# Kernel tuning notes

Measured on AMD Instinct MI355X. Metric: run time of the kernel, lower is better.

Reference implementation:

```python
import jax, jax.numpy as jnp
import numpy as np

EMB = 512      # emb_s * head_cnt = 64 * 8
EMB_S = 64     # scale uses sqrt(emb_s), not sqrt(emb) (quirk of source)
FF = 4 * EMB
LN_EPS = 1e-5


def layer_norm(x, g, b):
    mu = jnp.mean(x, axis=-1, keepdims=True)
    var = jnp.var(x, axis=-1, keepdims=True)
    return (x - mu) * jax.lax.rsqrt(var + LN_EPS) * g + b


def setup_inputs() -> dict:
    key = jax.random.key(0)
    ks = jax.random.split(key, 12)
    B, T = 512, 128
    s = 1.0 / np.sqrt(EMB)
    sf = 1.0 / np.sqrt(FF)
    return {
        "x": jax.random.normal(ks[0], (B, T, EMB), dtype=jnp.float32),
        "wq": jax.random.normal(ks[1], (EMB, EMB), dtype=jnp.float32) * s,
        "bq": jnp.zeros((EMB,), jnp.float32),
        "wk": jax.random.normal(ks[2], (EMB, EMB), dtype=jnp.float32) * s,
        "bk": jnp.zeros((EMB,), jnp.float32),
        "wv": jax.random.normal(ks[3], (EMB, EMB), dtype=jnp.float32) * s,
        "bv": jnp.zeros((EMB,), jnp.float32),
        "g1": jnp.ones((EMB,), jnp.float32),
        "b1": jnp.zeros((EMB,), jnp.float32),
        "g2": jnp.ones((EMB,), jnp.float32),
        "b2": jnp.zeros((EMB,), jnp.float32),
        "w1": jax.random.normal(ks[4], (EMB, FF), dtype=jnp.float32) * s,
        "bm1": jnp.zeros((FF,), jnp.float32),
        "w2": jax.random.normal(ks[5], (FF, EMB), dtype=jnp.float32) * sf,
        "bm2": jnp.zeros((EMB,), jnp.float32),
    }


def reference(x, wq, bq, wk, bk, wv, bv, g1, b1, g2, b2, w1, bm1, w2, bm2):
    B, T, E = x.shape
    # --- attention sub-block (single-head over full emb, per source forward) ---
    h = layer_norm(x, g1, b1)
    q = h @ wq + bq          # [B,T,E]
    k = h @ wk + bk
    v = h @ wv + bv
    att = jnp.einsum("bte,bse->bts", q, k) * (1.0 / np.sqrt(EMB_S))
    causal = jnp.tril(jnp.ones((T, T), dtype=bool))
    att = jnp.where(causal[None, :, :], att, -jnp.inf)
    att = jax.nn.softmax(att, axis=-1)
    y = jnp.einsum("bts,bse->bte", att, v)
    x = x + y  # note: no output projection / dropout on the forward path
    # --- MLP sub-block (dropout is identity in eval) ---
    h2 = layer_norm(x, g2, b2)
    m = jax.nn.gelu(h2 @ w1 + bm1, approximate=False) @ w2 + bm2
    return x + m
```

## Files before the change

kernel.cpp:

```cpp
#include <hip/hip_runtime.h>
#include <hip/hip_bf16.h>
#include <math.h>

typedef __attribute__((ext_vector_type(8))) short s16x8;
typedef __attribute__((ext_vector_type(4))) float f32x4;

static __device__ __forceinline__ float b2f(unsigned short u) {
    union { unsigned int u; float f; } x; x.u = ((unsigned int)u) << 16; return x.f;
}
static __device__ __forceinline__ unsigned short f2b(float f) {
    __hip_bfloat16 h = __float2bfloat16(f);
    return *reinterpret_cast<unsigned short*>(&h);
}
static __device__ __forceinline__ float gelu_fast(float x) {
    float s = x * fmaf(x * x, 0.07135481242f, 1.5957691216f);
    float e = __expf(-s);
    return x * __builtin_amdgcn_rcpf(1.0f + e);
}
static __device__ __forceinline__ void gload16(void* lds, const void* g) {
    __builtin_amdgcn_global_load_lds(
        (const __attribute__((address_space(1))) unsigned int*)g,
        (__attribute__((address_space(3))) unsigned int*)lds, 16, 0, 0);
}

__global__ __launch_bounds__(256) void cvt_t_kernel(
    const float* __restrict__ W, unsigned short* __restrict__ Wt, int K, int N)
{
    __shared__ unsigned short tile[32][33];
    int n0 = blockIdx.x * 32, k0 = blockIdx.y * 32;
    int tx = threadIdx.x & 31, ty = threadIdx.x >> 5;
#pragma unroll
    for (int p = 0; p < 32; p += 8)
        tile[tx][ty + p] = f2b(W[(size_t)(k0 + ty + p) * N + n0 + tx]);
    __syncthreads();
#pragma unroll
    for (int p = 0; p < 32; p += 8)
        Wt[(size_t)(n0 + ty + p) * K + k0 + tx] = tile[ty + p][tx];
}

__global__ __launch_bounds__(256) void concat3_kernel(
    const float* __restrict__ a, const float* __restrict__ b,
    const float* __restrict__ c, float* __restrict__ o)
{
    int i = blockIdx.x * 256 + threadIdx.x;
    if (i < 512) { o[i] = a[i]; o[512 + i] = b[i]; o[1024 + i] = c[i]; }
}

__global__ __launch_bounds__(256) void ln_kernel(
    const float* __restrict__ x,
    const float* __restrict__ g,
    const float* __restrict__ b,
    unsigned short* __restrict__ out, int rows)
{
    int row  = blockIdx.x * 4 + (threadIdx.x >> 6);
    int lane = threadIdx.x & 63;
    if (row >= rows) return;
    const float* xr = x + (size_t)row * 512 + lane * 8;
    float4 d0 = *(const float4*)xr;
    float4 d1 = *(const float4*)(xr + 4);
    float v[8] = {d0.x, d0.y, d0.z, d0.w, d1.x, d1.y, d1.z, d1.w};
    float s = 0.f, ss = 0.f;
#pragma unroll
    for (int j = 0; j < 8; ++j) { s += v[j]; ss += v[j] * v[j]; }
#pragma unroll
    for (int o = 32; o > 0; o >>= 1) { s += __shfl_xor(s, o); ss += __shfl_xor(ss, o); }
    float mu   = s * (1.0f / 512.0f);
    float var  = ss * (1.0f / 512.0f) - mu * mu;
    var = fmaxf(var, 0.0f);
    float rstd = rsqrtf(var + 1e-5f);
    float4 g0 = *(const float4*)(g + lane * 8);
    float4 g1 = *(const float4*)(g + lane * 8 + 4);
    float4 b0 = *(const float4*)(b + lane * 8);
    float4 b1 = *(const float4*)(b + lane * 8 + 4);
    float gg[8] = {g0.x, g0.y, g0.z, g0.w, g1.x, g1.y, g1.z, g1.w};
    float bb[8] = {b0.x, b0.y, b0.z, b0.w, b1.x, b1.y, b1.z, b1.w};
    uint4 res; unsigned short* rs = (unsigned short*)&res;
#pragma unroll
    for (int j = 0; j < 8; ++j)
        rs[j] = f2b((v[j] - mu) * rstd * gg[j] + bb[j]);
    *(uint4*)(out + (size_t)row * 512 + lane * 8) = res;
}

__global__ __launch_bounds__(256) void gemm_bt_kernel(
    const unsigned short* __restrict__ A,
    const unsigned short* __restrict__ Bt,
    const float* __restrict__ bias,
    const float* __restrict__ residual,
    void* __restrict__ Cv,
    int M, int N, int K, int act_gelu, int out_f32)
{
    __shared__ unsigned short As[128 * 32];
    __shared__ unsigned short Bs[128 * 32];

    const int tid  = threadIdx.x;
    const int wave = tid >> 6, lane = tid & 63;
    const int quad = lane >> 4, l16 = lane & 15;

    int bx = blockIdx.x, by = blockIdx.y;
    {
        int nwg = gridDim.x * gridDim.y;
        if ((nwg & 7) == 0) {
            int lid = by * gridDim.x + bx;
            int cpx = nwg >> 3;
            lid = (lid & 7) * cpx + (lid >> 3);
            bx = lid % gridDim.x;
            by = lid / gridDim.x;
        }
    }
    const int bm = by * 128, bn = bx * 128;
    const int wm = (wave >> 1) * 64, wn = (wave & 1) * 64;

    const int srow = 16 * wave + (lane >> 2);
    const int sgrp = (lane & 3) ^ ((srow >> 1) & 3);
    const unsigned short* a_src = A  + (size_t)(bm + srow) * K + sgrp * 8;
    const unsigned short* b_src = Bt + (size_t)(bn + srow) * K + sgrp * 8;
    const size_t rowskip = (size_t)64 * K;
    unsigned short* ldsA = As + 512 * wave;
    unsigned short* ldsB = Bs + 512 * wave;

    const int axor = ((quad ^ ((l16 >> 1) & 3)) * 8);

    f32x4 acc[4][4] = {};

    for (int k0 = 0; k0 < K; k0 += 32) {
        gload16(ldsA,        a_src + k0);
        gload16(ldsA + 2048, a_src + rowskip + k0);
        gload16(ldsB,        b_src + k0);
        gload16(ldsB + 2048, b_src + rowskip + k0);
        __syncthreads();

        s16x8 af[4], bfr[4];
#pragma unroll
        for (int i = 0; i < 4; ++i)
            af[i] = *(const s16x8*)&As[(wm + i * 16 + l16) * 32 + axor];
#pragma unroll
        for (int j = 0; j < 4; ++j)
            bfr[j] = *(const s16x8*)&Bs[(wn + j * 16 + l16) * 32 + axor];
#pragma unroll
        for (int i = 0; i < 4; ++i)
#pragma unroll
            for (int j = 0; j < 4; ++j)
                acc[i][j] = __builtin_amdgcn_mfma_f32_16x16x32_bf16(af[i], bfr[j], acc[i][j], 0, 0, 0);
        __syncthreads();
    }

#pragma unroll
    for (int i = 0; i < 4; ++i) {
#pragma unroll
        for (int j = 0; j < 4; ++j) {
#pragma unroll
            for (int r = 0; r < 4; ++r) {
                int row = bm + wm + i * 16 + quad * 4 + r;
                int col = bn + wn + j * 16 + l16;
                float val = acc[i][j][r] + bias[col];
                if (act_gelu) val = gelu_fast(val);
                if (residual) val += residual[(size_t)row * N + col];
                if (out_f32) ((float*)Cv)[(size_t)row * N + col] = val;
                else ((unsigned short*)Cv)[(size_t)row * N + col] = f2b(val);
            }
        }
    }
}

__global__ __launch_bounds__(256) void attn_kernel(
    const unsigned short* __restrict__ qkv,
    const float* __restrict__ x,
    float* __restrict__ x2)
{
    __shared__ unsigned short Ps[128][128];
    __shared__ unsigned short Vs[64][128];

    int b = blockIdx.x;
    int tid = threadIdx.x;
    int wave = tid >> 6, lane = tid & 63;
    int quad = lane >> 4, l16 = lane & 15;
    const unsigned short* qb = qkv + (size_t)b * 128 * 1536;
    const size_t bo = (size_t)b * 128 * 512;

    f32x4 acc[2][8] = {};
    for (int e0 = 0; e0 < 512; e0 += 32) {
        s16x8 a0 = *(const s16x8*)(qb + (size_t)(wave * 32 + l16) * 1536 + e0 + quad * 8);
        s16x8 a1 = *(const s16x8*)(qb + (size_t)(wave * 32 + 16 + l16) * 1536 + e0 + quad * 8);
#pragma unroll
        for (int j = 0; j < 8; ++j) {
            s16x8 bf = *(const s16x8*)(qb + (size_t)(j * 16 + l16) * 1536 + 512 + e0 + quad * 8);
            acc[0][j] = __builtin_amdgcn_mfma_f32_16x16x32_bf16(a0, bf, acc[0][j], 0, 0, 0);
            acc[1][j] = __builtin_amdgcn_mfma_f32_16x16x32_bf16(a1, bf, acc[1][j], 0, 0, 0);
        }
    }

    const float NEG = -1e30f;
#pragma unroll
    for (int i = 0; i < 2; ++i) {
#pragma unroll
        for (int r = 0; r < 4; ++r) {
            int t = wave * 32 + i * 16 + quad * 4 + r;
            float m = NEG;
#pragma unroll
            for (int j = 0; j < 8; ++j) {
                int s_col = j * 16 + l16;
                float val = acc[i][j][r] * 0.125f;
                val = (s_col <= t) ? val : NEG;
                acc[i][j][r] = val;
                m = fmaxf(m, val);
            }
            for (int o = 1; o < 16; o <<= 1) m = fmaxf(m, __shfl_xor(m, o));
            float sm = 0.f;
#pragma unroll
            for (int j = 0; j < 8; ++j) {
                float e = __expf(acc[i][j][r] - m);
                acc[i][j][r] = e;
                sm += e;
            }
            for (int o = 1; o < 16; o <<= 1) sm += __shfl_xor(sm, o);
            float inv = 1.0f / sm;
#pragma unroll
            for (int j = 0; j < 8; ++j) {
                int g = (j * 2 + (l16 >> 3)) ^ (t & 7);
                Ps[t][g * 8 + (l16 & 7)] = f2b(acc[i][j][r] * inv);
            }
        }
    }
    __syncthreads();

    const float* xb = x + bo;
    float* ob = x2 + bo;
    for (int e0 = 0; e0 < 512; e0 += 64) {
        if (e0) __syncthreads();
#pragma unroll
        for (int p = 0; p < 4; ++p) {
            int s = (tid >> 3) + p * 32;
            int c = (tid & 7) * 8;
            uint4 d = *(const uint4*)(qb + (size_t)s * 1536 + 1024 + e0 + c);
            const unsigned short* dsv = (const unsigned short*)&d;
#pragma unroll
            for (int j = 0; j < 8; ++j) {
                int rr = c + j;
                int g = (s >> 3) ^ j ^ (tid & 7);
                Vs[rr][g * 8 + (s & 7)] = dsv[j];
            }
        }
        __syncthreads();

        f32x4 acc2[2][4] = {};
#pragma unroll
        for (int ks = 0; ks < 4; ++ks) {
            int gp = ((ks * 4 + quad) ^ (l16 & 7)) * 8;
            s16x8 a0 = *(const s16x8*)(&Ps[wave * 32 + l16][gp]);
            s16x8 a1 = *(const s16x8*)(&Ps[wave * 32 + 16 + l16][gp]);
#pragma unroll
            for (int n = 0; n < 4; ++n) {
                int gv = ((ks * 4 + quad) ^ (l16 & 7) ^ ((2 * n + (l16 >> 3)) & 7)) * 8;
                s16x8 bf = *(const s16x8*)(&Vs[n * 16 + l16][gv]);
                acc2[0][n] = __builtin_amdgcn_mfma_f32_16x16x32_bf16(a0, bf, acc2[0][n], 0, 0, 0);
                acc2[1][n] = __builtin_amdgcn_mfma_f32_16x16x32_bf16(a1, bf, acc2[1][n], 0, 0, 0);
            }
        }
#pragma unroll
        for (int i = 0; i < 2; ++i) {
#pragma unroll
            for (int n = 0; n < 4; ++n) {
#pragma unroll
                for (int r = 0; r < 4; ++r) {
                    int t = wave * 32 + i * 16 + quad * 4 + r;
                    int e = e0 + n * 16 + l16;
                    ob[(size_t)t * 512 + e] = acc2[i][n][r] + xb[(size_t)t * 512 + e];
                }
            }
        }
    }
}

extern "C" void kernel_launch(void* const* d_in, const int* in_sizes, int n_in,
                              void* d_out, int out_size, void* d_ws, size_t ws_size,
                              hipStream_t stream) {
    const float* x   = (const float*)d_in[0];
    const float* wq  = (const float*)d_in[1];
    const float* bq  = (const float*)d_in[2];
    const float* wk  = (const float*)d_in[3];
    const float* bk  = (const float*)d_in[4];
    const float* wv  = (const float*)d_in[5];
    const float* bv  = (const float*)d_in[6];
    const float* g1  = (const float*)d_in[7];
    const float* b1  = (const float*)d_in[8];
    const float* g2  = (const float*)d_in[9];
    const float* b2  = (const float*)d_in[10];
    const float* w1  = (const float*)d_in[11];
    const float* bm1 = (const float*)d_in[12];
    const float* w2  = (const float*)d_in[13];
    const float* bm2 = (const float*)d_in[14];
    float* out = (float*)d_out;

    const int BATCH = 512, T = 128;
    dim3 blk(256);

    unsigned short* wqt = (unsigned short*)d_ws;
    unsigned short* wkt = wqt + 262144;
    unsigned short* wvt = wkt + 262144;
    unsigned short* w1t = wvt + 262144;
    unsigned short* w2t = w1t + 1048576;
    float* bqkv = (float*)(w2t + 1048576);
    cvt_t_kernel<<<dim3(16, 16), blk, 0, stream>>>(wq, wqt, 512, 512);
    cvt_t_kernel<<<dim3(16, 16), blk, 0, stream>>>(wk, wkt, 512, 512);
    cvt_t_kernel<<<dim3(16, 16), blk, 0, stream>>>(wv, wvt, 512, 512);
    cvt_t_kernel<<<dim3(64, 16), blk, 0, stream>>>(w1, w1t, 512, 2048);
    cvt_t_kernel<<<dim3(16, 64), blk, 0, stream>>>(w2, w2t, 2048, 512);
    concat3_kernel<<<dim3(2), blk, 0, stream>>>(bq, bk, bv, bqkv);

    int C = 512;
    while (C > 1 && 5773312ull + (size_t)C * 917504ull > ws_size) C >>= 1;

    const int R = C * T;
    const size_t S = (size_t)R * 512;
    char* dyn = (char*)(bqkv + 1536);
    unsigned short* h   = (unsigned short*)dyn;
    float*          x2f = (float*)(dyn + S * 2);
    unsigned short* qkv = (unsigned short*)(dyn + S * 2 + S * 4);
    unsigned short* mff = qkv;

    for (int b0 = 0; b0 < BATCH; b0 += C) {
        const size_t off = (size_t)b0 * T * 512;
        ln_kernel<<<R / 4, blk, 0, stream>>>(x + off, g1, b1, h, R);
        gemm_bt_kernel<<<dim3(12, R / 128), blk, 0, stream>>>(h, wqt, bqkv, nullptr, qkv, R, 1536, 512, 0, 0);
        attn_kernel<<<C, blk, 0, stream>>>(qkv, x + off, x2f);
        ln_kernel<<<R / 4, blk, 0, stream>>>(x2f, g2, b2, h, R);
        gemm_bt_kernel<<<dim3(16, R / 128), blk, 0, stream>>>(h, w1t, bm1, nullptr, mff, R, 2048, 512, 1, 0);
        gemm_bt_kernel<<<dim3(4, R / 128), blk, 0, stream>>>(mff, w2t, bm2, x2f, out + off, R, 512, 2048, 0, 1);
    }
}
```

Before: 1.162 ms.

## Multi-buffer LDS tiles in GEMM with prefetch two stages ahead

```diff
diff --git a/kernel.cpp b/kernel.cpp
--- a/kernel.cpp
+++ b/kernel.cpp
@@ -89,8 +89,8 @@
     void* __restrict__ Cv,
     int M, int N, int K, int act_gelu, int out_f32)
 {
-    __shared__ unsigned short As[128 * 32];
-    __shared__ unsigned short Bs[128 * 32];
+    __shared__ unsigned short As[4][128 * 32];
+    __shared__ unsigned short Bs[4][128 * 32];
 
     const int tid  = threadIdx.x;
     const int wave = tid >> 6, lane = tid & 63;
@@ -115,34 +115,55 @@
     const unsigned short* a_src = A  + (size_t)(bm + srow) * K + sgrp * 8;
     const unsigned short* b_src = Bt + (size_t)(bn + srow) * K + sgrp * 8;
     const size_t rowskip = (size_t)64 * K;
-    unsigned short* ldsA = As + 512 * wave;
-    unsigned short* ldsB = Bs + 512 * wave;
+    const int wo = 512 * wave;
 
     const int axor = ((quad ^ ((l16 >> 1) & 3)) * 8);
 
     f32x4 acc[4][4] = {};
 
-    for (int k0 = 0; k0 < K; k0 += 32) {
-        gload16(ldsA,        a_src + k0);
-        gload16(ldsA + 2048, a_src + rowskip + k0);
-        gload16(ldsB,        b_src + k0);
-        gload16(ldsB + 2048, b_src + rowskip + k0);
-        __syncthreads();
-
+    const int nt = K >> 5;
+
+    gload16(As[0] + wo,        a_src);
+    gload16(As[0] + wo + 2048, a_src + rowskip);
+    gload16(Bs[0] + wo,        b_src);
+    gload16(Bs[0] + wo + 2048, b_src + rowskip);
+    gload16(As[1] + wo,        a_src + 32);
+    gload16(As[1] + wo + 2048, a_src + rowskip + 32);
+    gload16(Bs[1] + wo,        b_src + 32);
+    gload16(Bs[1] + wo + 2048, b_src + rowskip + 32);
+
+    for (int t = 0; t < nt; ++t) {
+        asm volatile("s_waitcnt vmcnt(4)" ::: "memory");
+        __builtin_amdgcn_s_barrier();
+        __builtin_amdgcn_sched_barrier(0);
+
+        const unsigned short* Ar = As[t & 3];
+        const unsigned short* Br = Bs[t & 3];
         s16x8 af[4], bfr[4];
 #pragma unroll
         for (int i = 0; i < 4; ++i)
-            af[i] = *(const s16x8*)&As[(wm + i * 16 + l16) * 32 + axor];
+            af[i] = *(const s16x8*)&Ar[(wm + i * 16 + l16) * 32 + axor];
 #pragma unroll
         for (int j = 0; j < 4; ++j)
-            bfr[j] = *(const s16x8*)&Bs[(wn + j * 16 + l16) * 32 + axor];
+            bfr[j] = *(const s16x8*)&Br[(wn + j * 16 + l16) * 32 + axor];
+
+        {
+            int kp = (t + 2 < nt) ? ((t + 2) << 5) : 0;
+            unsigned short* Aw = As[(t + 2) & 3];
+            unsigned short* Bw = Bs[(t + 2) & 3];
+            gload16(Aw + wo,        a_src + kp);
+            gload16(Aw + wo + 2048, a_src + rowskip + kp);
+            gload16(Bw + wo,        b_src + kp);
+            gload16(Bw + wo + 2048, b_src + rowskip + kp);
+        }
+
 #pragma unroll
         for (int i = 0; i < 4; ++i)
 #pragma unroll
             for (int j = 0; j < 4; ++j)
                 acc[i][j] = __builtin_amdgcn_mfma_f32_16x16x32_bf16(af[i], bfr[j], acc[i][j], 0, 0, 0);
-        __syncthreads();
-    }
+    }
+    asm volatile("s_waitcnt vmcnt(0)" ::: "memory");
 
 #pragma unroll
     for (int i = 0; i < 4; ++i) {
```

Result: slower. 1.197 ms (+3.0%).

## Rewrite GEMM as 256x256 tile, 8-wave double-buffered pipelined kernel

Applied to the files above, without the earlier changes.

```diff
diff --git a/kernel.cpp b/kernel.cpp
--- a/kernel.cpp
+++ b/kernel.cpp
@@ -81,7 +81,7 @@
     *(uint4*)(out + (size_t)row * 512 + lane * 8) = res;
 }
 
-__global__ __launch_bounds__(256) void gemm_bt_kernel(
+__global__ __launch_bounds__(512, 2) void gemm_bt_kernel(
     const unsigned short* __restrict__ A,
     const unsigned short* __restrict__ Bt,
     const float* __restrict__ bias,
@@ -89,12 +89,12 @@
     void* __restrict__ Cv,
     int M, int N, int K, int act_gelu, int out_f32)
 {
-    __shared__ unsigned short As[128 * 32];
-    __shared__ unsigned short Bs[128 * 32];
+    __shared__ unsigned short Lds[2][2][2][256][32];
 
     const int tid  = threadIdx.x;
-    const int wave = tid >> 6, lane = tid & 63;
+    const int w    = tid >> 6, lane = tid & 63;
     const int quad = lane >> 4, l16 = lane & 15;
+    const int wm8  = w >> 2, wn8 = w & 3;
 
     int bx = blockIdx.x, by = blockIdx.y;
     {
@@ -107,52 +107,123 @@
             by = lid / gridDim.x;
         }
     }
-    const int bm = by * 128, bn = bx * 128;
-    const int wm = (wave >> 1) * 64, wn = (wave & 1) * 64;
-
-    const int srow = 16 * wave + (lane >> 2);
-    const int sgrp = (lane & 3) ^ ((srow >> 1) & 3);
-    const unsigned short* a_src = A  + (size_t)(bm + srow) * K + sgrp * 8;
-    const unsigned short* b_src = Bt + (size_t)(bn + srow) * K + sgrp * 8;
-    const size_t rowskip = (size_t)64 * K;
-    unsigned short* ldsA = As + 512 * wave;
-    unsigned short* ldsB = Bs + 512 * wave;
-
-    const int axor = ((quad ^ ((l16 >> 1) & 3)) * 8);
-
-    f32x4 acc[4][4] = {};
-
-    for (int k0 = 0; k0 < K; k0 += 32) {
-        gload16(ldsA,        a_src + k0);
-        gload16(ldsA + 2048, a_src + rowskip + k0);
-        gload16(ldsB,        b_src + k0);
-        gload16(ldsB + 2048, b_src + rowskip + k0);
-        __syncthreads();
-
-        s16x8 af[4], bfr[4];
-#pragma unroll
-        for (int i = 0; i < 4; ++i)
-            af[i] = *(const s16x8*)&As[(wm + i * 16 + l16) * 32 + axor];
-#pragma unroll
-        for (int j = 0; j < 4; ++j)
-            bfr[j] = *(const s16x8*)&Bs[(wn + j * 16 + l16) * 32 + axor];
-#pragma unroll
-        for (int i = 0; i < 4; ++i)
-#pragma unroll
-            for (int j = 0; j < 4; ++j)
-                acc[i][j] = __builtin_amdgcn_mfma_f32_16x16x32_bf16(af[i], bfr[j], acc[i][j], 0, 0, 0);
-        __syncthreads();
-    }
-
-#pragma unroll
-    for (int i = 0; i < 4; ++i) {
-#pragma unroll
-        for (int j = 0; j < 4; ++j) {
+    const int bm = by * 256, bn = bx * 256;
+
+    const int srow = w * 16 + (lane >> 2);
+    const int sg   = (lane & 3) ^ ((lane >> 3) & 3);
+    const unsigned short* a_src = A  + (size_t)(bm + srow) * K + sg * 8;
+    const unsigned short* b_src = Bt + (size_t)(bn + srow) * K + sg * 8;
+    const size_t cskip = (size_t)128 * K;
+
+    const int axor = (quad ^ ((l16 >> 1) & 3)) * 8;
+
+    f32x4 acc[8][4] = {};
+
+    const int nt = K >> 6;
+
+    auto STG = [&](int buf, int op, int kh, int kt) {
+        const unsigned short* src = op ? b_src : a_src;
+        const int ko = kt * 64 + kh * 32;
+        gload16(&Lds[buf][op][kh][w * 16][0],       src + ko);
+        gload16(&Lds[buf][op][kh][128 + w * 16][0], src + cskip + ko);
+    };
+
+    STG(0, 0, 0, 0); STG(0, 1, 0, 0); STG(0, 0, 1, 0); STG(0, 1, 1, 0);
+    asm volatile("s_waitcnt vmcnt(4)" ::: "memory");
+    __builtin_amdgcn_s_barrier();
+
+    for (int t = 0; t < nt; ++t) {
+        const int buf = t & 1, nb = buf ^ 1;
+        const int ktn = (t + 1 < nt) ? t + 1 : 0;
+        s16x8 a4[4], b4[4];
+
+#pragma unroll
+        for (int m = 0; m < 4; ++m)
+            a4[m] = *(const s16x8*)&Lds[buf][0][0][wm8 * 128 + m * 16 + l16][axor];
+#pragma unroll
+        for (int n = 0; n < 4; ++n)
+            b4[n] = *(const s16x8*)&Lds[buf][1][0][wn8 * 64 + n * 16 + l16][axor];
+        STG(nb, 0, 0, ktn);
+        __builtin_amdgcn_sched_barrier(0);
+        __builtin_amdgcn_s_barrier();
+        __builtin_amdgcn_sched_barrier(0);
+        __builtin_amdgcn_s_setprio(1);
+#pragma unroll
+        for (int m = 0; m < 4; ++m)
+#pragma unroll
+            for (int n = 0; n < 4; ++n)
+                acc[m][n] = __builtin_amdgcn_mfma_f32_16x16x32_bf16(a4[m], b4[n], acc[m][n], 0, 0, 0);
+        __builtin_amdgcn_s_setprio(0);
+        __builtin_amdgcn_sched_barrier(0);
+        __builtin_amdgcn_s_barrier();
+
+#pragma unroll
+        for (int m = 0; m < 4; ++m)
+            a4[m] = *(const s16x8*)&Lds[buf][0][0][wm8 * 128 + (m + 4) * 16 + l16][axor];
+        STG(nb, 1, 0, ktn);
+        __builtin_amdgcn_sched_barrier(0);
+        __builtin_amdgcn_s_barrier();
+        __builtin_amdgcn_sched_barrier(0);
+        __builtin_amdgcn_s_setprio(1);
+#pragma unroll
+        for (int m = 0; m < 4; ++m)
+#pragma unroll
+            for (int n = 0; n < 4; ++n)
+                acc[m + 4][n] = __builtin_amdgcn_mfma_f32_16x16x32_bf16(a4[m], b4[n], acc[m + 4][n], 0, 0, 0);
+        __builtin_amdgcn_s_setprio(0);
+        asm volatile("s_waitcnt vmcnt(4)" ::: "memory");
+        __builtin_amdgcn_sched_barrier(0);
+        __builtin_amdgcn_s_barrier();
+
+#pragma unroll
+        for (int m = 0; m < 4; ++m)
+            a4[m] = *(const s16x8*)&Lds[buf][0][1][wm8 * 128 + m * 16 + l16][axor];
+#pragma unroll
+        for (int n = 0; n < 4; ++n)
+            b4[n] = *(const s16x8*)&Lds[buf][1][1][wn8 * 64 + n * 16 + l16][axor];
+        STG(nb, 0, 1, ktn);
+        __builtin_amdgcn_sched_barrier(0);
+        __builtin_amdgcn_s_barrier();
+        __builtin_amdgcn_sched_barrier(0);
+        __builtin_amdgcn_s_setprio(1);
+#pragma unroll
+        for (int m = 0; m < 4; ++m)
+#pragma unroll
+            for (int n = 0; n < 4; ++n)
+                acc[m][n] = __builtin_amdgcn_mfma_f32_16x16x32_bf16(a4[m], b4[n], acc[m][n], 0, 0, 0);
+        __builtin_amdgcn_s_setprio(0);
+        __builtin_amdgcn_sched_barrier(0);
+        __builtin_amdgcn_s_barrier();
+
+#pragma unroll
+        for (int m = 0; m < 4; ++m)
+            a4[m] = *(const s16x8*)&Lds[buf][0][1][wm8 * 128 + (m + 4) * 16 + l16][axor];
+        STG(nb, 1, 1, ktn);
+        __builtin_amdgcn_sched_barrier(0);
+        __builtin_amdgcn_s_barrier();
+        __builtin_amdgcn_sched_barrier(0);
+        __builtin_amdgcn_s_setprio(1);
+#pragma unroll
+        for (int m = 0; m < 4; ++m)
+#pragma unroll
+            for (int n = 0; n < 4; ++n)
+                acc[m + 4][n] = __builtin_amdgcn_mfma_f32_16x16x32_bf16(a4[m], b4[n], acc[m + 4][n], 0, 0, 0);
+        __builtin_amdgcn_s_setprio(0);
+        asm volatile("s_waitcnt vmcnt(4)" ::: "memory");
+        __builtin_amdgcn_sched_barrier(0);
+        __builtin_amdgcn_s_barrier();
+    }
+    asm volatile("s_waitcnt vmcnt(0)" ::: "memory");
+
+#pragma unroll
+    for (int m = 0; m < 8; ++m) {
+#pragma unroll
+        for (int n = 0; n < 4; ++n) {
 #pragma unroll
             for (int r = 0; r < 4; ++r) {
-                int row = bm + wm + i * 16 + quad * 4 + r;
-                int col = bn + wn + j * 16 + l16;
-                float val = acc[i][j][r] + bias[col];
+                int row = bm + wm8 * 128 + m * 16 + quad * 4 + r;
+                int col = bn + wn8 * 64 + n * 16 + l16;
+                float val = acc[m][n][r] + bias[col];
                 if (act_gelu) val = gelu_fast(val);
                 if (residual) val += residual[(size_t)row * N + col];
                 if (out_f32) ((float*)Cv)[(size_t)row * N + col] = val;
@@ -292,7 +363,7 @@
     float* out = (float*)d_out;
 
     const int BATCH = 512, T = 128;
-    dim3 blk(256);
+    dim3 blk(256), blkg(512);
 
     unsigned short* wqt = (unsigned short*)d_ws;
     unsigned short* wkt = wqt + 262144;
@@ -308,7 +379,7 @@
     concat3_kernel<<<dim3(2), blk, 0, stream>>>(bq, bk, bv, bqkv);
 
     int C = 512;
-    while (C > 1 && 5773312ull + (size_t)C * 917504ull > ws_size) C >>= 1;
+    while (C > 4 && 5773312ull + (size_t)C * 917504ull > ws_size) C >>= 1;
 
     const int R = C * T;
     const size_t S = (size_t)R * 512;
@@ -321,10 +392,10 @@
     for (int b0 = 0; b0 < BATCH; b0 += C) {
         const size_t off = (size_t)b0 * T * 512;
         ln_kernel<<<R / 4, blk, 0, stream>>>(x + off, g1, b1, h, R);
-        gemm_bt_kernel<<<dim3(12, R / 128), blk, 0, stream>>>(h, wqt, bqkv, nullptr, qkv, R, 1536, 512, 0, 0);
+        gemm_bt_kernel<<<dim3(6, R / 256), blkg, 0, stream>>>(h, wqt, bqkv, nullptr, qkv, R, 1536, 512, 0, 0);
         attn_kernel<<<C, blk, 0, stream>>>(qkv, x + off, x2f);
         ln_kernel<<<R / 4, blk, 0, stream>>>(x2f, g2, b2, h, R);
-        gemm_bt_kernel<<<dim3(16, R / 128), blk, 0, stream>>>(h, w1t, bm1, nullptr, mff, R, 2048, 512, 1, 0);
-        gemm_bt_kernel<<<dim3(4, R / 128), blk, 0, stream>>>(mff, w2t, bm2, x2f, out + off, R, 512, 2048, 0, 1);
-    }
-}
+        gemm_bt_kernel<<<dim3(8, R / 256), blkg, 0, stream>>>(h, w1t, bm1, nullptr, mff, R, 2048, 512, 1, 0);
+        gemm_bt_kernel<<<dim3(2, R / 256), blkg, 0, stream>>>(mff, w2t, bm2, x2f, out + off, R, 512, 2048, 0, 1);
+    }
+}
```

Result: faster. 1.050 ms (-9.7%).

## Triple-buffer GEMM LDS loads with 256x128 tiles and 8-wave blocks

Applied to the files above, without the earlier changes.

```diff
diff --git a/kernel.cpp b/kernel.cpp
--- a/kernel.cpp
+++ b/kernel.cpp
@@ -81,7 +81,7 @@
     *(uint4*)(out + (size_t)row * 512 + lane * 8) = res;
 }
 
-__global__ __launch_bounds__(256) void gemm_bt_kernel(
+__global__ __launch_bounds__(512, 4) void gemm_bt_kernel(
     const unsigned short* __restrict__ A,
     const unsigned short* __restrict__ Bt,
     const float* __restrict__ bias,
@@ -89,12 +89,13 @@
     void* __restrict__ Cv,
     int M, int N, int K, int act_gelu, int out_f32)
 {
-    __shared__ unsigned short As[128 * 32];
-    __shared__ unsigned short Bs[128 * 32];
+    __shared__ unsigned short LA[3][256][32];
+    __shared__ unsigned short LB[3][128][32];
 
     const int tid  = threadIdx.x;
-    const int wave = tid >> 6, lane = tid & 63;
+    const int w    = tid >> 6, lane = tid & 63;
     const int quad = lane >> 4, l16 = lane & 15;
+    const int wm   = (w >> 1) * 64, wn = (w & 1) * 64;
 
     int bx = blockIdx.x, by = blockIdx.y;
     {
@@ -107,52 +108,71 @@
             by = lid / gridDim.x;
         }
     }
-    const int bm = by * 128, bn = bx * 128;
-    const int wm = (wave >> 1) * 64, wn = (wave & 1) * 64;
-
-    const int srow = 16 * wave + (lane >> 2);
-    const int sgrp = (lane & 3) ^ ((srow >> 1) & 3);
-    const unsigned short* a_src = A  + (size_t)(bm + srow) * K + sgrp * 8;
-    const unsigned short* b_src = Bt + (size_t)(bn + srow) * K + sgrp * 8;
-    const size_t rowskip = (size_t)64 * K;
-    unsigned short* ldsA = As + 512 * wave;
-    unsigned short* ldsB = Bs + 512 * wave;
-
-    const int axor = ((quad ^ ((l16 >> 1) & 3)) * 8);
+    const int bm = by * 256, bn = bx * 128;
+
+    const int srow = w * 16 + (lane >> 2);
+    const int sg   = (lane & 3) ^ ((lane >> 3) & 3);
+    const unsigned short* a_src = A  + (size_t)(bm + srow) * K + sg * 8;
+    const unsigned short* b_src = Bt + (size_t)(bn + srow) * K + sg * 8;
+    const size_t a_skip = (size_t)128 * K;
+
+    const int axor = (quad ^ ((l16 >> 1) & 3)) * 8;
 
     f32x4 acc[4][4] = {};
-
-    for (int k0 = 0; k0 < K; k0 += 32) {
-        gload16(ldsA,        a_src + k0);
-        gload16(ldsA + 2048, a_src + rowskip + k0);
-        gload16(ldsB,        b_src + k0);
-        gload16(ldsB + 2048, b_src + rowskip + k0);
-        __syncthreads();
-
-        s16x8 af[4], bfr[4];
-#pragma unroll
-        for (int i = 0; i < 4; ++i)
-            af[i] = *(const s16x8*)&As[(wm + i * 16 + l16) * 32 + axor];
-#pragma unroll
-        for (int j = 0; j < 4; ++j)
-            bfr[j] = *(const s16x8*)&Bs[(wn + j * 16 + l16) * 32 + axor];
-#pragma unroll
-        for (int i = 0; i < 4; ++i)
-#pragma unroll
-            for (int j = 0; j < 4; ++j)
-                acc[i][j] = __builtin_amdgcn_mfma_f32_16x16x32_bf16(af[i], bfr[j], acc[i][j], 0, 0, 0);
-        __syncthreads();
-    }
-
-#pragma unroll
-    for (int i = 0; i < 4; ++i) {
-#pragma unroll
-        for (int j = 0; j < 4; ++j) {
+    const int nt = K >> 5;
+
+    auto STG = [&](int sb, int kt) {
+        const int ko = kt << 5;
+        gload16(&LA[sb][w * 16][0],       a_src + ko);
+        gload16(&LA[sb][128 + w * 16][0], a_src + a_skip + ko);
+        gload16(&LB[sb][w * 16][0],       b_src + ko);
+    };
+
+    STG(0, 0);
+    STG(1, 1);
+    asm volatile("s_waitcnt vmcnt(3)" ::: "memory");
+    __builtin_amdgcn_s_barrier();
+
+    int cur = 0, stg = 2;
+    for (int t = 0; t < nt; ++t) {
+        s16x8 a4[4], b4[4];
+#pragma unroll
+        for (int m = 0; m < 4; ++m)
+            a4[m] = *(const s16x8*)&LA[cur][wm + m * 16 + l16][axor];
+#pragma unroll
+        for (int n = 0; n < 4; ++n)
+            b4[n] = *(const s16x8*)&LB[cur][wn + n * 16 + l16][axor];
+
+        STG(stg, (t + 2 < nt) ? t + 2 : 0);
+        asm volatile("s_waitcnt vmcnt(3)" ::: "memory");
+        __builtin_amdgcn_sched_barrier(0);
+        __builtin_amdgcn_s_barrier();
+        __builtin_amdgcn_sched_barrier(0);
+
+        __builtin_amdgcn_s_setprio(1);
+#pragma unroll
+        for (int m = 0; m < 4; ++m)
+#pragma unroll
+            for (int n = 0; n < 4; ++n)
+                acc[m][n] = __builtin_amdgcn_mfma_f32_16x16x32_bf16(a4[m], b4[n], acc[m][n], 0, 0, 0);
+        __builtin_amdgcn_s_setprio(0);
+        __builtin_amdgcn_sched_barrier(0);
+        __builtin_amdgcn_s_barrier();
+
+        cur = (cur == 2) ? 0 : cur + 1;
+        stg = (stg == 2) ? 0 : stg + 1;
+    }
+    asm volatile("s_waitcnt vmcnt(0)" ::: "memory");
+
+#pragma unroll
+    for (int m = 0; m < 4; ++m) {
+#pragma unroll
+        for (int n = 0; n < 4; ++n) {
 #pragma unroll
             for (int r = 0; r < 4; ++r) {
-                int row = bm + wm + i * 16 + quad * 4 + r;
-                int col = bn + wn + j * 16 + l16;
-                float val = acc[i][j][r] + bias[col];
+                int row = bm + wm + m * 16 + quad * 4 + r;
+                int col = bn + wn + n * 16 + l16;
+                float val = acc[m][n][r] + bias[col];
                 if (act_gelu) val = gelu_fast(val);
                 if (residual) val += residual[(size_t)row * N + col];
                 if (out_f32) ((float*)Cv)[(size_t)row * N + col] = val;
@@ -292,7 +312,7 @@
     float* out = (float*)d_out;
 
     const int BATCH = 512, T = 128;
-    dim3 blk(256);
+    dim3 blk(256), blkg(512);
 
     unsigned short* wqt = (unsigned short*)d_ws;
     unsigned short* wkt = wqt + 262144;
@@ -308,7 +328,7 @@
     concat3_kernel<<<dim3(2), blk, 0, stream>>>(bq, bk, bv, bqkv);
 
     int C = 512;
-    while (C > 1 && 5773312ull + (size_t)C * 917504ull > ws_size) C >>= 1;
+    while (C > 8 && 5773312ull + (size_t)C * 917504ull > ws_size) C >>= 1;
 
     const int R = C * T;
     const size_t S = (size_t)R * 512;
@@ -321,10 +341,10 @@
     for (int b0 = 0; b0 < BATCH; b0 += C) {
         const size_t off = (size_t)b0 * T * 512;
         ln_kernel<<<R / 4, blk, 0, stream>>>(x + off, g1, b1, h, R);
-        gemm_bt_kernel<<<dim3(12, R / 128), blk, 0, stream>>>(h, wqt, bqkv, nullptr, qkv, R, 1536, 512, 0, 0);
+        gemm_bt_kernel<<<dim3(12, R / 256), blkg, 0, stream>>>(h, wqt, bqkv, nullptr, qkv, R, 1536, 512, 0, 0);
         attn_kernel<<<C, blk, 0, stream>>>(qkv, x + off, x2f);
         ln_kernel<<<R / 4, blk, 0, stream>>>(x2f, g2, b2, h, R);
-        gemm_bt_kernel<<<dim3(16, R / 128), blk, 0, stream>>>(h, w1t, bm1, nullptr, mff, R, 2048, 512, 1, 0);
-        gemm_bt_kernel<<<dim3(4, R / 128), blk, 0, stream>>>(mff, w2t, bm2, x2f, out + off, R, 512, 2048, 0, 1);
-    }
-}
+        gemm_bt_kernel<<<dim3(16, R / 256), blkg, 0, stream>>>(h, w1t, bm1, nullptr, mff, R, 2048, 512, 1, 0);
+        gemm_bt_kernel<<<dim3(4, R / 256), blkg, 0, stream>>>(mff, w2t, bm2, x2f, out + off, R, 512, 2048, 0, 1);
+    }
+}
```

Result: faster. 1.024 ms (-11.9%).
